# Optimization experiments

Measured on AMD Instinct MI355X. Metric: run time of the kernel, lower is better.

Reference implementation:

```python
import jax, jax.numpy as jnp
import numpy as np

B, T, C, H, WINDOW = 256, 1024, 128, 256, 24


def setup_inputs() -> dict:
    key = jax.random.key(0)
    ks = jax.random.split(key, 9)
    s = 1.0 / np.sqrt(H)  # torch LSTMCell uniform init scale
    return {
        "x": jax.random.normal(ks[0], (B, T, C), dtype=jnp.float32),
        "W_ih": jax.random.uniform(ks[1], (4 * H, C), jnp.float32, -s, s),
        "W_hh": jax.random.uniform(ks[2], (4 * H, H), jnp.float32, -s, s),
        "b_ih": jax.random.uniform(ks[3], (4 * H,), jnp.float32, -s, s),
        "b_hh": jax.random.uniform(ks[4], (4 * H,), jnp.float32, -s, s),
        "W_skip": jax.random.normal(ks[5], (H, H), dtype=jnp.float32) * np.sqrt(2.0 / (H + H)),
        "b_skip": jnp.zeros((H,), jnp.float32),
        "h0": jax.random.normal(ks[6], (1, H), dtype=jnp.float32) * np.sqrt(2.0 / (1 + H)),
        "c0": jax.random.normal(ks[7], (1, H), dtype=jnp.float32) * np.sqrt(2.0 / (1 + H)),
    }


def reference(x, W_ih, W_hh, b_ih, b_hh, W_skip, b_skip, h0, c0):
    Bb, Tt, _ = x.shape
    Hh = h0.shape[1]
    h = jnp.tile(h0, (Bb, 1))
    c = jnp.tile(c0, (Bb, 1))
    # ring buffer of the last WINDOW hidden states (output[i-WINDOW] lives at slot i % WINDOW)
    buf = jnp.zeros((WINDOW, Bb, Hh), x.dtype)
    # precompute the input contribution to the gates for all timesteps: [T, B, 4H]
    xg = jnp.einsum('btc,gc->tbg', x, W_ih) + b_ih + b_hh

    def step(carry, inp):
        h, c, buf = carry
        xg_t, i = inp
        idx = i % WINDOW
        skip = jax.lax.dynamic_index_in_dim(buf, idx, 0, keepdims=False)  # output[i-WINDOW]
        mask = (i >= WINDOW).astype(x.dtype)
        h_in = h + mask * (skip @ W_skip.T + b_skip)
        gates = xg_t + h_in @ W_hh.T  # [B, 4H]
        gi, gf, gg, go = jnp.split(gates, 4, axis=-1)  # torch order: i, f, g, o
        c_new = jax.nn.sigmoid(gf) * c + jax.nn.sigmoid(gi) * jnp.tanh(gg)
        h_new = jax.nn.sigmoid(go) * jnp.tanh(c_new)
        buf = jax.lax.dynamic_update_index_in_dim(buf, h_new, idx, 0)
        return (h_new, c_new, buf), h_new

    (h, c, _), out = jax.lax.scan(step, (h, c, buf), (xg, jnp.arange(Tt)))
    output = jnp.swapaxes(out, 0, 1)  # [B, T, H]
    return output, h, c
```

## Files before the change

kernel.cpp:

```cpp
#include <hip/hip_runtime.h>
#include <cstddef>

#define Bn  256
#define Tn  1024
#define Cn  128
#define Hn  256
#define WIN 24

#define NRG 16
#define NUG 8
#define RPB 16
#define UPB 32

#define AGENT __HIP_MEMORY_SCOPE_AGENT
#define RLX   __ATOMIC_RELAXED

typedef __attribute__((ext_vector_type(8))) short bf16x8;
typedef __attribute__((ext_vector_type(4))) float f32x4;

#define MFMA(a, b, c) __builtin_amdgcn_mfma_f32_16x16x32_bf16((a), (b), (c), 0, 0, 0)

struct __align__(64) Flag { int v; int pad[15]; };
__device__ Flag g_flag[NRG][NUG];
__device__ unsigned short g_hx_hi[2][Bn][Hn];
__device__ unsigned short g_hx_lo[2][Bn][Hn];

__device__ inline unsigned short f2bf(float f) {
    union { float f; unsigned u; } v; v.f = f;
    unsigned r = (v.u + 0x7FFF + ((v.u >> 16) & 1)) >> 16;
    return (unsigned short)r;
}
__device__ inline float bf2f(unsigned short b) {
    union { unsigned u; float f; } v; v.u = (unsigned)b << 16;
    return v.f;
}
__device__ inline void split8(const float* s, bf16x8& hi, bf16x8& lo) {
    #pragma unroll
    for (int e = 0; e < 8; ++e) {
        unsigned short h = f2bf(s[e]);
        float r = s[e] - bf2f(h);
        hi[e] = (short)h;
        lo[e] = (short)f2bf(r);
    }
}
__device__ inline float fsigm(float x) {
    return __builtin_amdgcn_rcpf(1.f + exp2f(x * -1.442695041f));
}
__device__ inline float ftanh(float x) {
    return 1.f - 2.f * __builtin_amdgcn_rcpf(1.f + exp2f(x * 2.885390082f));
}

__global__ __launch_bounds__(256) void init_sync(const float* __restrict__ h0) {
    int i = blockIdx.x * 256 + threadIdx.x;
    int b = i >> 8, u = i & 255;
    float hv = h0[u];
    unsigned short hi = f2bf(hv);
    g_hx_hi[0][b][u] = hi;
    g_hx_lo[0][b][u] = f2bf(hv - bf2f(hi));
    g_hx_hi[1][b][u] = 0;
    g_hx_lo[1][b][u] = 0;
    if (i < NRG * NUG) ((Flag*)g_flag)[i].v = 0;
}

__global__ __launch_bounds__(512, 1) void lstm_persist(
    const float* __restrict__ x,
    const float* __restrict__ W_ih, const float* __restrict__ W_hh,
    const float* __restrict__ b_ih, const float* __restrict__ b_hh,
    const float* __restrict__ W_skip, const float* __restrict__ b_skip,
    const float* __restrict__ h0, const float* __restrict__ c0,
    float* __restrict__ outp, float* __restrict__ hbuf, float* __restrict__ cbuf)
{
    __shared__ bf16x8 s_ga[2][12][64];
    __shared__ bf16x8 s_sa[2][8][64];
    __shared__ float  s_part[8][64][4];
    __shared__ float  s_sk[4][2][64][4];
    __shared__ __align__(16) unsigned short s_hown_hi[16][32];
    __shared__ __align__(16) unsigned short s_hown_lo[16][32];
    __shared__ float  s_hout[16][32];
    __shared__ float  s_bias[128];
    __shared__ float  s_bskip[UPB];
    __shared__ float  s_pad[5000];

    const int tid = threadIdx.x;
    if (tid == 0) ((volatile float*)s_pad)[0] = 0.f;

    const int xcd = blockIdx.x & 7, slot = blockIdx.x >> 3;
    const int rg = (xcd << 1) | (slot >> 3), ug = slot & 7;
    const int row0 = rg * RPB, u0 = ug * UPB;

    const int w = tid >> 6, lane = tid & 63;
    const int g  = w >> 1, uh = w & 1;
    const int nl = lane & 15, kq = lane >> 4;
    const int sm = lane & 15;
    const int k0 = w * 32 + kq * 8;
    const bool own = (w == ug);
    const int cm = tid >> 5, cu = tid & 31;
    const int cli = ((cm >> 2) << 4) | (cu & 15), cr = cm & 3, cuh = cu >> 4;
    const int ksx2 = w - 4;
    const int mx2 = lane & 15, kqx2 = lane >> 4;

    bf16x8 whh_hi[8], whh_lo[8], wx_hi[4], wx_lo[4], ws_hi[2], ws_lo[2];
    {
        const int Rg = g * Hn + u0 + uh * 16 + nl;
        const float* wr = W_hh + (size_t)Rg * Hn;
        #pragma unroll
        for (int j = 0; j < 8; ++j) {
            float tmp[8];
            const int k = j * 32 + kq * 8;
            #pragma unroll
            for (int e = 0; e < 8; ++e) tmp[e] = wr[k + e];
            split8(tmp, whh_hi[j], whh_lo[j]);
        }
        const float* wr2 = W_ih + (size_t)Rg * Cn;
        #pragma unroll
        for (int j = 0; j < 4; ++j) {
            float tmp[8];
            const int k = j * 32 + kq * 8;
            #pragma unroll
            for (int e = 0; e < 8; ++e) tmp[e] = wr2[k + e];
            split8(tmp, wx_hi[j], wx_lo[j]);
        }
        const int Rs = u0 + uh * 16 + nl;
        const float* wr3 = W_skip + (size_t)Rs * Hn;
        #pragma unroll
        for (int j = 0; j < 2; ++j) {
            float tmp[8];
            const int k = ((w >> 1) * 2 + j) * 32 + kq * 8;
            #pragma unroll
            for (int e = 0; e < 8; ++e) tmp[e] = wr3[k + e];
            split8(tmp, ws_hi[j], ws_lo[j]);
        }
    }
    if (tid < 128) s_bias[tid] = b_ih[(tid >> 5) * Hn + u0 + (tid & 31)]
                               + b_hh[(tid >> 5) * Hn + u0 + (tid & 31)];
    if (tid < UPB) s_bskip[tid] = b_skip[u0 + tid];

    float c_reg = c0[u0 + cu];
    {
        float hv = h0[u0 + cu];
        unsigned short phi = f2bf(hv);
        s_hown_hi[cm][cu] = phi;
        s_hown_lo[cm][cu] = f2bf(hv - bf2f(phi));
    }
    if (tid < 256) {
        const int ksx = tid >> 6;
        const float* src = x + (size_t)(row0 + sm) * (Tn * Cn) + ksx * 32 + kq * 8;
        float tmp[8];
        #pragma unroll
        for (int e = 0; e < 8; ++e) tmp[e] = src[e];
        bf16x8 hi, lo; split8(tmp, hi, lo);
        s_ga[0][ksx][lane] = hi; s_ga[1][ksx][lane] = lo;
    }
    f32x4 ring_a = {0.f,0.f,0.f,0.f}, ring_b = {0.f,0.f,0.f,0.f};
    __syncthreads();

    for (int t = 0; t < Tn; ++t) {
        const bool do_ring = (t >= WIN - 1) && (t < Tn - 1);
        const bool nr      = (t >= WIN - 2) && (t < Tn - 2);
        const int  par     = t & 1;

        int fv = 0x7fffffff;
        if (!own) fv = __hip_atomic_load(&g_flag[rg][w].v, RLX, AGENT);

        if (do_ring) {
            asm volatile("s_waitcnt vmcnt(0)" : "+v"(ring_a), "+v"(ring_b) :: "memory");
            float rvv[8];
            #pragma unroll
            for (int e = 0; e < 4; ++e) { rvv[e] = ring_a[e]; rvv[4 + e] = ring_b[e]; }
            bf16x8 hi, lo; split8(rvv, hi, lo);
            s_sa[0][w][lane] = hi; s_sa[1][w][lane] = lo;
        }
        __syncthreads();

        const unsigned short* hip_ = &g_hx_hi[par][row0 + sm][k0];
        const unsigned short* lop_ = &g_hx_lo[par][row0 + sm][k0];
        bf16x8 ha, hb;
        bool have = false;
        if (!own && fv >= t) {
            have = true;
            asm volatile("global_load_dwordx4 %0, %2, off sc0 sc1\n\t"
                         "global_load_dwordx4 %1, %3, off sc0 sc1"
                         : "=&v"(ha), "=&v"(hb) : "v"(hip_), "v"(lop_) : "memory");
        }

        f32x4 ac0 = {0.f,0.f,0.f,0.f}, ac1 = {0.f,0.f,0.f,0.f}, ac2 = {0.f,0.f,0.f,0.f};
        #pragma unroll
        for (int j = 0; j < 4; ++j) {
            bf16x8 ah = s_ga[0][j][lane], al = s_ga[1][j][lane];
            ac0 = MFMA(ah, wx_hi[j], ac0);
            ac1 = MFMA(ah, wx_lo[j], ac1);
            ac2 = MFMA(al, wx_hi[j], ac2);
        }
        if (do_ring) {
            f32x4 sk0 = {0.f,0.f,0.f,0.f}, sk1 = {0.f,0.f,0.f,0.f}, sk2 = {0.f,0.f,0.f,0.f};
            #pragma unroll
            for (int j = 0; j < 2; ++j) {
                const int ks = (w >> 1) * 2 + j;
                bf16x8 ah = s_sa[0][ks][lane], al = s_sa[1][ks][lane];
                sk0 = MFMA(ah, ws_hi[j], sk0);
                sk1 = MFMA(ah, ws_lo[j], sk1);
                sk2 = MFMA(al, ws_hi[j], sk2);
            }
            *(f32x4*)&s_sk[w >> 1][w & 1][lane][0] = sk0 + sk1 + sk2;
        }
        if (!own && !have) {
            fv = __hip_atomic_load(&g_flag[rg][w].v, RLX, AGENT);
            if (fv >= t) {
                have = true;
                asm volatile("global_load_dwordx4 %0, %2, off sc0 sc1\n\t"
                             "global_load_dwordx4 %1, %3, off sc0 sc1"
                             : "=&v"(ha), "=&v"(hb) : "v"(hip_), "v"(lop_) : "memory");
            }
        }

        if (!own) {
            while (fv < t)
                fv = __hip_atomic_load(&g_flag[rg][w].v, RLX, AGENT);
            if (!have) {
                asm volatile("global_load_dwordx4 %0, %2, off sc0 sc1\n\t"
                             "global_load_dwordx4 %1, %3, off sc0 sc1"
                             : "=&v"(ha), "=&v"(hb) : "v"(hip_), "v"(lop_) : "memory");
            }
            asm volatile("s_waitcnt vmcnt(0)" : "+v"(ha), "+v"(hb) :: "memory");
            s_ga[0][4 + w][lane] = ha;
            s_ga[1][4 + w][lane] = hb;
        } else {
            s_ga[0][4 + w][lane] = *(const bf16x8*)&s_hown_hi[sm][kq * 8];
            s_ga[1][4 + w][lane] = *(const bf16x8*)&s_hown_lo[sm][kq * 8];
        }
        if (nr) {
            const float* rsrc = outp + (size_t)(row0 + sm) * (Tn * Hn)
                                     + (size_t)(t - (WIN - 2)) * Hn + k0;
            asm volatile("global_load_dwordx4 %0, %2, off sc0 sc1\n\t"
                         "global_load_dwordx4 %1, %2, off offset:16 sc0 sc1"
                         : "=&v"(ring_a), "=&v"(ring_b) : "v"(rsrc) : "memory");
        }
        f32x4 xa, xb;
        const bool xst = (w >= 4) && (t + 1 < Tn);
        if (xst) {
            const float* xsrc = x + (size_t)(row0 + mx2) * (Tn * Cn)
                                  + (size_t)(t + 1) * Cn + ksx2 * 32 + kqx2 * 8;
            xa = *(const f32x4*)xsrc;
            xb = *(const f32x4*)(xsrc + 4);
        }
        __syncthreads();

        #pragma unroll
        for (int j = 0; j < 8; ++j) {
            bf16x8 ah = s_ga[0][4 + j][lane], al = s_ga[1][4 + j][lane];
            ac0 = MFMA(ah, whh_hi[j], ac0);
            ac1 = MFMA(ah, whh_lo[j], ac1);
            ac2 = MFMA(al, whh_hi[j], ac2);
        }
        *(f32x4*)&s_part[w][lane][0] = ac0 + ac1 + ac2;
        __syncthreads();

        {
            float gv[4];
            #pragma unroll
            for (int g2 = 0; g2 < 4; ++g2)
                gv[g2] = s_part[g2 * 2 + cuh][cli][cr] + s_bias[g2 * 32 + cu];
            float si = fsigm(gv[0]);
            float sf = fsigm(gv[1]);
            float gt = ftanh(gv[2]);
            float so = fsigm(gv[3]);
            c_reg = sf * c_reg + si * gt;
            float hn = so * ftanh(c_reg);
            s_hout[cm][cu] = hn;
            if (t < Tn - 1) {
                float hin = hn;
                if (do_ring) {
                    float sk = s_sk[0][cuh][cli][cr] + s_sk[1][cuh][cli][cr]
                             + s_sk[2][cuh][cli][cr] + s_sk[3][cuh][cli][cr];
                    hin += sk + s_bskip[cu];
                }
                unsigned short phi = f2bf(hin);
                s_hown_hi[cm][cu] = phi;
                s_hown_lo[cm][cu] = f2bf(hin - bf2f(phi));
            } else {
                hbuf[(size_t)(row0 + cm) * Hn + u0 + cu] = hn;
                cbuf[(size_t)(row0 + cm) * Hn + u0 + cu] = c_reg;
            }
        }
        __syncthreads();

        if (tid < 64) {
            if (t < Tn - 1) {
                const int r8 = lane >> 2, q = lane & 3;
                f32x4 vh = *(const f32x4*)&s_hown_hi[r8][q * 8];
                f32x4 vl = *(const f32x4*)&s_hown_lo[r8][q * 8];
                unsigned short* dh = &g_hx_hi[par ^ 1][row0 + r8][u0 + q * 8];
                unsigned short* dl = &g_hx_lo[par ^ 1][row0 + r8][u0 + q * 8];
                asm volatile("global_store_dwordx4 %0, %2, off sc0 sc1\n\t"
                             "global_store_dwordx4 %1, %3, off sc0 sc1"
                             :: "v"(dh), "v"(dl), "v"(vh), "v"(vl) : "memory");
                asm volatile("s_waitcnt vmcnt(0)" ::: "memory");
                if (lane == 0)
                    __hip_atomic_store(&g_flag[rg][ug].v, t + 1, RLX, AGENT);
            }
        } else if (tid < 192) {
            const int i = tid - 64, r8 = i >> 3, q = i & 7;
            f32x4 v = *(const f32x4*)&s_hout[r8][q * 4];
            float* dst = &outp[(size_t)(row0 + r8) * (Tn * Hn) + (size_t)t * Hn + u0 + q * 4];
            asm volatile("global_store_dwordx4 %0, %1, off sc0 sc1"
                         :: "v"(dst), "v"(v) : "memory");
        } else if (xst) {
            float tmp[8];
            #pragma unroll
            for (int e = 0; e < 4; ++e) { tmp[e] = xa[e]; tmp[4 + e] = xb[e]; }
            bf16x8 hi, lo; split8(tmp, hi, lo);
            s_ga[0][ksx2][lane] = hi;
            s_ga[1][ksx2][lane] = lo;
        }
    }
}

extern "C" void kernel_launch(void* const* d_in, const int* in_sizes, int n_in,
                              void* d_out, int out_size, void* d_ws, size_t ws_size,
                              hipStream_t stream)
{
    const float* x      = (const float*)d_in[0];
    const float* W_ih   = (const float*)d_in[1];
    const float* W_hh   = (const float*)d_in[2];
    const float* b_ih   = (const float*)d_in[3];
    const float* b_hh   = (const float*)d_in[4];
    const float* W_skip = (const float*)d_in[5];
    const float* b_skip = (const float*)d_in[6];
    const float* h0     = (const float*)d_in[7];
    const float* c0     = (const float*)d_in[8];

    float* outp = (float*)d_out;
    float* hbuf = outp + (size_t)Bn * Tn * Hn;
    float* cbuf = hbuf + (size_t)Bn * Hn;

    init_sync<<<256, 256, 0, stream>>>(h0);
    lstm_persist<<<128, 512, 0, stream>>>(x, W_ih, W_hh, b_ih, b_hh,
                                          W_skip, b_skip, h0, c0, outp, hbuf, cbuf);
}
```

Before: 3.377 ms.

## Publish hidden state per wave with packed hi/lo and counter-based sync

The hi and lo bf16 halves of the exchanged hidden state are packed into one 32-bit word. Every consumer thread now stores its own h value and output element straight to global memory, which removes the trailing __syncthreads and the single wave that used to stage and publish the data. Readiness becomes a counter that each of the 8 waves increments with an atomic add, and consumers wait until it reaches 8*t. In exchange, global stores become scattered dword writes instead of dwordx4, and consumers need extra bit shuffling to unpack the halves.

```diff
diff --git a/kernel.cpp b/kernel.cpp
--- a/kernel.cpp
+++ b/kernel.cpp
@@ -17,13 +17,13 @@
 
 typedef __attribute__((ext_vector_type(8))) short bf16x8;
 typedef __attribute__((ext_vector_type(4))) float f32x4;
+typedef __attribute__((ext_vector_type(4))) unsigned int u32x4;
 
 #define MFMA(a, b, c) __builtin_amdgcn_mfma_f32_16x16x32_bf16((a), (b), (c), 0, 0, 0)
 
-struct __align__(64) Flag { int v; int pad[15]; };
-__device__ Flag g_flag[NRG][NUG];
-__device__ unsigned short g_hx_hi[2][Bn][Hn];
-__device__ unsigned short g_hx_lo[2][Bn][Hn];
+struct __align__(64) Ctr { int v; int pad[15]; };
+__device__ Ctr g_ctr[NRG][NUG];
+__device__ unsigned g_hx_pk[2][Bn][Hn];
 
 __device__ inline unsigned short f2bf(float f) {
     union { float f; unsigned u; } v; v.f = f;
@@ -55,11 +55,10 @@
     int b = i >> 8, u = i & 255;
     float hv = h0[u];
     unsigned short hi = f2bf(hv);
-    g_hx_hi[0][b][u] = hi;
-    g_hx_lo[0][b][u] = f2bf(hv - bf2f(hi));
-    g_hx_hi[1][b][u] = 0;
-    g_hx_lo[1][b][u] = 0;
-    if (i < NRG * NUG) ((Flag*)g_flag)[i].v = 0;
+    unsigned short lo = f2bf(hv - bf2f(hi));
+    g_hx_pk[0][b][u] = ((unsigned)hi << 16) | lo;
+    g_hx_pk[1][b][u] = 0;
+    if (i < NRG * NUG) ((Ctr*)g_ctr)[i].v = 0;
 }
 
 __global__ __launch_bounds__(512, 1) void lstm_persist(
@@ -76,10 +75,9 @@
     __shared__ float  s_sk[4][2][64][4];
     __shared__ __align__(16) unsigned short s_hown_hi[16][32];
     __shared__ __align__(16) unsigned short s_hown_lo[16][32];
-    __shared__ float  s_hout[16][32];
     __shared__ float  s_bias[128];
     __shared__ float  s_bskip[UPB];
-    __shared__ float  s_pad[5000];
+    __shared__ float  s_pad[5600];
 
     const int tid = threadIdx.x;
     if (tid == 0) ((volatile float*)s_pad)[0] = 0.f;
@@ -158,9 +156,10 @@
         const bool do_ring = (t >= WIN - 1) && (t < Tn - 1);
         const bool nr      = (t >= WIN - 2) && (t < Tn - 2);
         const int  par     = t & 1;
+        const int  need    = 8 * t;
 
         int fv = 0x7fffffff;
-        if (!own) fv = __hip_atomic_load(&g_flag[rg][w].v, RLX, AGENT);
+        if (!own) fv = __hip_atomic_load(&g_ctr[rg][w].v, RLX, AGENT);
 
         if (do_ring) {
             asm volatile("s_waitcnt vmcnt(0)" : "+v"(ring_a), "+v"(ring_b) :: "memory");
@@ -172,15 +171,14 @@
         }
         __syncthreads();
 
-        const unsigned short* hip_ = &g_hx_hi[par][row0 + sm][k0];
-        const unsigned short* lop_ = &g_hx_lo[par][row0 + sm][k0];
-        bf16x8 ha, hb;
+        const unsigned* pkp = &g_hx_pk[par][row0 + sm][k0];
+        u32x4 pa = {0,0,0,0}, pb = {0,0,0,0};
         bool have = false;
-        if (!own && fv >= t) {
+        if (!own && fv >= need) {
             have = true;
             asm volatile("global_load_dwordx4 %0, %2, off sc0 sc1\n\t"
-                         "global_load_dwordx4 %1, %3, off sc0 sc1"
-                         : "=&v"(ha), "=&v"(hb) : "v"(hip_), "v"(lop_) : "memory");
+                         "global_load_dwordx4 %1, %2, off offset:16 sc0 sc1"
+                         : "=&v"(pa), "=&v"(pb) : "v"(pkp) : "memory");
         }
 
         f32x4 ac0 = {0.f,0.f,0.f,0.f}, ac1 = {0.f,0.f,0.f,0.f}, ac2 = {0.f,0.f,0.f,0.f};
@@ -204,26 +202,34 @@
             *(f32x4*)&s_sk[w >> 1][w & 1][lane][0] = sk0 + sk1 + sk2;
         }
         if (!own && !have) {
-            fv = __hip_atomic_load(&g_flag[rg][w].v, RLX, AGENT);
-            if (fv >= t) {
+            fv = __hip_atomic_load(&g_ctr[rg][w].v, RLX, AGENT);
+            if (fv >= need) {
                 have = true;
                 asm volatile("global_load_dwordx4 %0, %2, off sc0 sc1\n\t"
-                             "global_load_dwordx4 %1, %3, off sc0 sc1"
-                             : "=&v"(ha), "=&v"(hb) : "v"(hip_), "v"(lop_) : "memory");
+                             "global_load_dwordx4 %1, %2, off offset:16 sc0 sc1"
+                             : "=&v"(pa), "=&v"(pb) : "v"(pkp) : "memory");
             }
         }
 
         if (!own) {
-            while (fv < t)
-                fv = __hip_atomic_load(&g_flag[rg][w].v, RLX, AGENT);
+            while (fv < need)
+                fv = __hip_atomic_load(&g_ctr[rg][w].v, RLX, AGENT);
             if (!have) {
                 asm volatile("global_load_dwordx4 %0, %2, off sc0 sc1\n\t"
-                             "global_load_dwordx4 %1, %3, off sc0 sc1"
-                             : "=&v"(ha), "=&v"(hb) : "v"(hip_), "v"(lop_) : "memory");
-            }
-            asm volatile("s_waitcnt vmcnt(0)" : "+v"(ha), "+v"(hb) :: "memory");
-            s_ga[0][4 + w][lane] = ha;
-            s_ga[1][4 + w][lane] = hb;
+                             "global_load_dwordx4 %1, %2, off offset:16 sc0 sc1"
+                             : "=&v"(pa), "=&v"(pb) : "v"(pkp) : "memory");
+            }
+            asm volatile("s_waitcnt vmcnt(0)" : "+v"(pa), "+v"(pb) :: "memory");
+            union { bf16x8 v; unsigned d[4]; } Hh, Ll;
+            #pragma unroll
+            for (int e = 0; e < 2; ++e) {
+                Hh.d[e]     = (pa[2*e+1] & 0xFFFF0000u) | (pa[2*e] >> 16);
+                Ll.d[e]     = (pa[2*e+1] << 16)         | (pa[2*e] & 0xFFFFu);
+                Hh.d[2 + e] = (pb[2*e+1] & 0xFFFF0000u) | (pb[2*e] >> 16);
+                Ll.d[2 + e] = (pb[2*e+1] << 16)         | (pb[2*e] & 0xFFFFu);
+            }
+            s_ga[0][4 + w][lane] = Hh.v;
+            s_ga[1][4 + w][lane] = Ll.v;
         } else {
             s_ga[0][4 + w][lane] = *(const bf16x8*)&s_hown_hi[sm][kq * 8];
             s_ga[1][4 + w][lane] = *(const bf16x8*)&s_hown_lo[sm][kq * 8];
@@ -266,7 +272,9 @@
             float so = fsigm(gv[3]);
             c_reg = sf * c_reg + si * gt;
             float hn = so * ftanh(c_reg);
-            s_hout[cm][cu] = hn;
+            float* odst = &outp[(size_t)(row0 + cm) * (Tn * Hn) + (size_t)t * Hn + u0 + cu];
+            asm volatile("global_store_dword %0, %1, off sc0 sc1"
+                         :: "v"(odst), "v"(hn) : "memory");
             if (t < Tn - 1) {
                 float hin = hn;
                 if (do_ring) {
@@ -275,42 +283,32 @@
                     hin += sk + s_bskip[cu];
                 }
                 unsigned short phi = f2bf(hin);
+                unsigned short plo = f2bf(hin - bf2f(phi));
                 s_hown_hi[cm][cu] = phi;
-                s_hown_lo[cm][cu] = f2bf(hin - bf2f(phi));
+                s_hown_lo[cm][cu] = plo;
+                unsigned pk = ((unsigned)phi << 16) | plo;
+                unsigned* hdst = &g_hx_pk[par ^ 1][row0 + cm][u0 + cu];
+                asm volatile("global_store_dword %0, %1, off sc0 sc1"
+                             :: "v"(hdst), "v"(pk) : "memory");
             } else {
                 hbuf[(size_t)(row0 + cm) * Hn + u0 + cu] = hn;
                 cbuf[(size_t)(row0 + cm) * Hn + u0 + cu] = c_reg;
             }
         }
-        __syncthreads();
-
-        if (tid < 64) {
-            if (t < Tn - 1) {
-                const int r8 = lane >> 2, q = lane & 3;
-                f32x4 vh = *(const f32x4*)&s_hown_hi[r8][q * 8];
-                f32x4 vl = *(const f32x4*)&s_hown_lo[r8][q * 8];
-                unsigned short* dh = &g_hx_hi[par ^ 1][row0 + r8][u0 + q * 8];
-                unsigned short* dl = &g_hx_lo[par ^ 1][row0 + r8][u0 + q * 8];
-                asm volatile("global_store_dwordx4 %0, %2, off sc0 sc1\n\t"
-                             "global_store_dwordx4 %1, %3, off sc0 sc1"
-                             :: "v"(dh), "v"(dl), "v"(vh), "v"(vl) : "memory");
-                asm volatile("s_waitcnt vmcnt(0)" ::: "memory");
-                if (lane == 0)
-                    __hip_atomic_store(&g_flag[rg][ug].v, t + 1, RLX, AGENT);
-            }
-        } else if (tid < 192) {
-            const int i = tid - 64, r8 = i >> 3, q = i & 7;
-            f32x4 v = *(const f32x4*)&s_hout[r8][q * 4];
-            float* dst = &outp[(size_t)(row0 + r8) * (Tn * Hn) + (size_t)t * Hn + u0 + q * 4];
-            asm volatile("global_store_dwordx4 %0, %1, off sc0 sc1"
-                         :: "v"(dst), "v"(v) : "memory");
-        } else if (xst) {
+
+        if (xst) {
             float tmp[8];
             #pragma unroll
             for (int e = 0; e < 4; ++e) { tmp[e] = xa[e]; tmp[4 + e] = xb[e]; }
             bf16x8 hi, lo; split8(tmp, hi, lo);
             s_ga[0][ksx2][lane] = hi;
             s_ga[1][ksx2][lane] = lo;
+        }
+
+        if (t < Tn - 1) {
+            asm volatile("s_waitcnt vmcnt(0)" ::: "memory");
+            if (lane == 0)
+                __hip_atomic_fetch_add(&g_ctr[rg][ug].v, 1, RLX, AGENT);
         }
     }
 }
```

Result: slower. 4.279 ms (+26.7%).
